# Optimization experiments

Measured on AMD Instinct MI355X. Metric: run time of the kernel, lower is better.

The kernel has to match this reference:

```python
import jax, jax.numpy as jnp
import numpy as np

C = 1.0          # Poincare ball curvature (geoopt PoincareBall default)
EPS = 1e-15      # geoopt clamp epsilon for fp32
FEAT_DIM = 256
NUM_OUTCOME = 128
BATCH = 2048
INIT_EPS = 0.001


def _clamp_abs(x, eps=EPS):
    # keep sign, clamp magnitude away from zero (geoopt clamp_abs)
    s = jnp.where(x >= 0, 1.0, -1.0)
    return s * jnp.maximum(jnp.abs(x), eps)


def mobius_add(x, y, c=C):
    # geoopt _mobius_add with k = -c; x, y broadcastable [..., D]
    k = -c
    x2 = jnp.sum(x * x, axis=-1, keepdims=True)
    y2 = jnp.sum(y * y, axis=-1, keepdims=True)
    xy = jnp.sum(x * y, axis=-1, keepdims=True)
    num = (1.0 - 2.0 * k * xy - k * y2) * x + (1.0 + k * x2) * y
    denom = 1.0 - 2.0 * k * xy + (k * k) * x2 * y2
    return num / jnp.maximum(denom, EPS)


def expmap0(u, c=C):
    # tanh(sqrt(c)||u||) * u / (sqrt(c)||u||)
    sqrt_c = jnp.sqrt(c)
    un = jnp.maximum(jnp.linalg.norm(u, axis=-1, keepdims=True), EPS)
    return jnp.tanh(sqrt_c * un) * u / (sqrt_c * un)


def setup_inputs() -> dict:
    key = jax.random.key(0)
    k1, k2, k3 = jax.random.split(key, 3)
    # input scaled to lie comfortably inside the unit ball
    x = 0.1 * jax.random.normal(k1, (BATCH, FEAT_DIM), dtype=jnp.float32)
    point = INIT_EPS * jax.random.normal(k2, (NUM_OUTCOME, FEAT_DIM), dtype=jnp.float32)
    tangent = INIT_EPS * jax.random.normal(k3, (NUM_OUTCOME, FEAT_DIM), dtype=jnp.float32)
    return {"input": x, "point": point, "tangent": tangent}


def reference(input, point, tangent):
    sqrt_c = jnp.sqrt(jnp.asarray(C, input.dtype))
    x = input.reshape(-1, FEAT_DIM)                    # [B, D]
    p = expmap0(point)                                 # [K, D]
    # vectorized over all K classes at once (replaces python per-class loop)
    diff = mobius_add(-p[None, :, :], x[:, None, :])   # [B, K, D]
    diff_norm2 = jnp.maximum(jnp.sum(diff * diff, axis=-1), EPS)   # [B, K]
    sc_diff_a = jnp.sum(diff * tangent[None, :, :], axis=-1)       # [B, K] signed
    a_norm = jnp.linalg.norm(tangent, axis=-1)                     # [K]
    k = -C
    num = 2.0 * sc_diff_a
    denom = _clamp_abs((1.0 + k * diff_norm2) * a_norm[None, :])
    # arsin_k for k < 0: arcsinh(sqrt(c) * z) / sqrt(c)
    distance = jnp.arcsinh(sqrt_c * (num / denom)) / sqrt_c
    logits = distance * a_norm[None, :]                # scaled=True
    return logits                                      # [B, K]
```

## Files before the change

### kernel.cpp

```cpp
#include <hip/hip_runtime.h>
#include <math.h>


constexpr int D   = 256;
constexpr int BT  = 32;
constexpr int KT  = 32;
constexpr int S   = 264;
constexpr float EPS = 1e-15f;

typedef __attribute__((ext_vector_type(8))) short short8;
typedef __attribute__((ext_vector_type(4))) float f32x4;

__device__ __forceinline__ ushort f2bf(float f) {
    uint u = __float_as_uint(f);
    u += 0x7FFFu + ((u >> 16) & 1u);
    return (ushort)(u >> 16);
}
__device__ __forceinline__ ushort4 bf4(float4 v) {
    return make_ushort4(f2bf(v.x), f2bf(v.y), f2bf(v.z), f2bf(v.w));
}
__device__ __forceinline__ float dot4(float4 a, float4 b) {
    return a.x * b.x + a.y * b.y + a.z * b.z + a.w * b.w;
}

__device__ __forceinline__ float epilogue(float s_raw, float t_raw, float U2,
                                          float cc, float P2, float PA, float AN) {
    float s     = cc * s_raw;
    float alpha = 1.f - 2.f * s + U2;
    float beta  = 1.f - P2;
    float gamma = fmaxf(1.f - 2.f * s + P2 * U2, EPS);
    float rg    = __builtin_amdgcn_rcpf(gamma);
    float nn    = alpha * alpha * P2 - 2.f * alpha * beta * s + beta * beta * U2;
    float dn2   = fmaxf(nn * rg * rg, EPS);
    float sc    = (beta * t_raw - alpha * PA) * rg;
    float draw  = (1.f - dn2) * AN;
    float den   = (draw >= 0.f ? 1.f : -1.f) * fmaxf(fabsf(draw), EPS);
    float z     = 2.f * sc * __builtin_amdgcn_rcpf(den);
    float az    = fabsf(z);
    float r = __builtin_amdgcn_logf(az + __builtin_amdgcn_sqrtf(__builtin_fmaf(az, az, 1.f)))
              * 0.6931471805599453f;
    return (z >= 0.f ? r : -r) * AN;
}

__global__ __launch_bounds__(512, 2)
void poincare_mlr_kernel(const float* __restrict__ X,
                         const float* __restrict__ P,
                         const float* __restrict__ A,
                         float* __restrict__ out,
                         int K) {
    __shared__ ushort xs[BT * S];
    __shared__ ushort ps[KT * S];
    __shared__ ushort as_[KT * S];
    __shared__ float U2s[BT];
    __shared__ float kcc[KT], kP2[KT], kPA[KT], kAN[KT];

    const int tid = threadIdx.x;
    const int kb  = blockIdx.x & 3;
    const int bb  = blockIdx.x >> 2;
    const int b0g = bb * BT;
    const int k0g = kb * KT;

    {
        const int rx = tid >> 4, g = tid & 15;
        const float4* Xr = (const float4*)(X + (size_t)(b0g + rx) * D);
        const float4* Pr = (const float4*)(P + (size_t)(k0g + rx) * D);
        const float4* Ar = (const float4*)(A + (size_t)(k0g + rx) * D);
        float x2 = 0.f, n2 = 0.f, pa = 0.f, a2 = 0.f;
        #pragma unroll
        for (int t = 0; t < 4; ++t) {
            const int c = g + 16 * t;
            float4 vx = Xr[c];
            float4 vp = Pr[c];
            float4 va = Ar[c];
            x2 += dot4(vx, vx);
            n2 += dot4(vp, vp);
            pa += dot4(vp, va);
            a2 += dot4(va, va);
            *(ushort4*)&xs[rx * S + 4 * c]  = bf4(vx);
            *(ushort4*)&ps[rx * S + 4 * c]  = bf4(vp);
            *(ushort4*)&as_[rx * S + 4 * c] = bf4(va);
        }
        #pragma unroll
        for (int off = 8; off; off >>= 1) {
            x2 += __shfl_xor(x2, off, 16);
            n2 += __shfl_xor(n2, off, 16);
            pa += __shfl_xor(pa, off, 16);
            a2 += __shfl_xor(a2, off, 16);
        }
        if (g == 0) {
            U2s[rx] = x2;
            float un = fmaxf(__builtin_amdgcn_sqrtf(n2), EPS);
            float u2 = un * un;
            float cc = 1.f - u2 * (1.f / 3.f) + u2 * u2 * (2.f / 15.f);
            if (un > 0.04f) cc = tanhf(un) / un;
            kcc[rx] = cc;
            kP2[rx] = cc * cc * n2;
            kPA[rx] = cc * pa;
            kAN[rx] = __builtin_amdgcn_sqrtf(a2);
        }
    }
    __syncthreads();

    const int lane = tid & 63, wv = tid >> 6;
    const int wb = wv & 1, wk = (wv >> 1) & 1, jh = wv >> 2;
    const int m  = lane & 15, kq = lane >> 4;

    const ushort* xb = xs  + (size_t)(wb * 16 + m) * S + kq * 8;
    const ushort* pb = ps  + (size_t)(wk * 16 + m) * S + kq * 8;
    const ushort* ab = as_ + (size_t)(wk * 16 + m) * S + kq * 8;

    f32x4 accS = {0.f, 0.f, 0.f, 0.f};
    f32x4 accT = {0.f, 0.f, 0.f, 0.f};
    #pragma unroll
    for (int st = 0; st < 8; ++st) {
        short8 xa = *(const short8*)(xb + st * 32);
        short8 pf = *(const short8*)(pb + st * 32);
        short8 af = *(const short8*)(ab + st * 32);
        accS = __builtin_amdgcn_mfma_f32_16x16x32_bf16(xa, pf, accS, 0, 0, 0);
        accT = __builtin_amdgcn_mfma_f32_16x16x32_bf16(xa, af, accT, 0, 0, 0);
    }

    const float sA = jh ? accS[2] : accS[0];
    const float tA = jh ? accT[2] : accT[0];
    const float sB = jh ? accS[3] : accS[1];
    const float tB = jh ? accT[3] : accT[1];

    const int kloc = wk * 16 + m;
    const float cc = kcc[kloc], P2 = kP2[kloc], PA = kPA[kloc], AN = kAN[kloc];
    const int kg = k0g + kloc;
    const int r0 = wb * 16 + kq * 4 + jh * 2;

    out[(size_t)(b0g + r0) * K + kg]     = epilogue(sA, tA, U2s[r0],     cc, P2, PA, AN);
    out[(size_t)(b0g + r0 + 1) * K + kg] = epilogue(sB, tB, U2s[r0 + 1], cc, P2, PA, AN);
}

extern "C" void kernel_launch(void* const* d_in, const int* in_sizes, int n_in,
                              void* d_out, int out_size, void* d_ws, size_t ws_size,
                              hipStream_t stream) {
    const float* X = (const float*)d_in[0];
    const float* P = (const float*)d_in[1];
    const float* A = (const float*)d_in[2];
    float* out = (float*)d_out;

    const int B = in_sizes[0] / D;
    const int K = in_sizes[1] / D;

    dim3 grid((B / BT) * (K / KT));
    poincare_mlr_kernel<<<grid, dim3(512), 0, stream>>>(X, P, A, out, K);
}
```

Before: 10.18 us.

## Hoist global loads, use library bf16 conversion, and nontemporal output stores

```diff
diff --git a/kernel.cpp b/kernel.cpp
--- a/kernel.cpp
+++ b/kernel.cpp
@@ -1,4 +1,5 @@
 #include <hip/hip_runtime.h>
+#include <hip/hip_bf16.h>
 #include <math.h>
 
 
@@ -12,9 +13,9 @@
 typedef __attribute__((ext_vector_type(4))) float f32x4;
 
 __device__ __forceinline__ ushort f2bf(float f) {
-    uint u = __float_as_uint(f);
-    u += 0x7FFFu + ((u >> 16) & 1u);
-    return (ushort)(u >> 16);
+    union { __hip_bfloat16 h; ushort u; } cv;
+    cv.h = __float2bfloat16(f);
+    return cv.u;
 }
 __device__ __forceinline__ ushort4 bf4(float4 v) {
     return make_ushort4(f2bf(v.x), f2bf(v.y), f2bf(v.z), f2bf(v.w));
@@ -65,20 +66,27 @@
         const float4* Xr = (const float4*)(X + (size_t)(b0g + rx) * D);
         const float4* Pr = (const float4*)(P + (size_t)(k0g + rx) * D);
         const float4* Ar = (const float4*)(A + (size_t)(k0g + rx) * D);
+
+        float4 vx[4], vp[4], va[4];
+        #pragma unroll
+        for (int t = 0; t < 4; ++t) {
+            const int c = g + 16 * t;
+            vx[t] = Xr[c];
+            vp[t] = Pr[c];
+            va[t] = Ar[c];
+        }
+
         float x2 = 0.f, n2 = 0.f, pa = 0.f, a2 = 0.f;
         #pragma unroll
         for (int t = 0; t < 4; ++t) {
             const int c = g + 16 * t;
-            float4 vx = Xr[c];
-            float4 vp = Pr[c];
-            float4 va = Ar[c];
-            x2 += dot4(vx, vx);
-            n2 += dot4(vp, vp);
-            pa += dot4(vp, va);
-            a2 += dot4(va, va);
-            *(ushort4*)&xs[rx * S + 4 * c]  = bf4(vx);
-            *(ushort4*)&ps[rx * S + 4 * c]  = bf4(vp);
-            *(ushort4*)&as_[rx * S + 4 * c] = bf4(va);
+            x2 += dot4(vx[t], vx[t]);
+            n2 += dot4(vp[t], vp[t]);
+            pa += dot4(vp[t], va[t]);
+            a2 += dot4(va[t], va[t]);
+            *(ushort4*)&xs[rx * S + 4 * c]  = bf4(vx[t]);
+            *(ushort4*)&ps[rx * S + 4 * c]  = bf4(vp[t]);
+            *(ushort4*)&as_[rx * S + 4 * c] = bf4(va[t]);
         }
         #pragma unroll
         for (int off = 8; off; off >>= 1) {
@@ -130,8 +138,12 @@
     const int kg = k0g + kloc;
     const int r0 = wb * 16 + kq * 4 + jh * 2;
 
-    out[(size_t)(b0g + r0) * K + kg]     = epilogue(sA, tA, U2s[r0],     cc, P2, PA, AN);
-    out[(size_t)(b0g + r0 + 1) * K + kg] = epilogue(sB, tB, U2s[r0 + 1], cc, P2, PA, AN);
+    __builtin_nontemporal_store(
+        epilogue(sA, tA, U2s[r0], cc, P2, PA, AN),
+        &out[(size_t)(b0g + r0) * K + kg]);
+    __builtin_nontemporal_store(
+        epilogue(sB, tB, U2s[r0 + 1], cc, P2, PA, AN),
+        &out[(size_t)(b0g + r0 + 1) * K + kg]);
 }
 
 extern "C" void kernel_launch(void* const* d_in, const int* in_sizes, int n_in,
```

Result: slower. 11.76 us (+15.5%).
